# Kernel optimization log

Hardware: AMD Instinct MI355X
Metric: run time of the kernel (lower is better)

## Reference

```python
import jax, jax.numpy as jnp
import numpy as np

B, T, H, PRED = 16384, 8, 256, 12


def _cell(x, h, c, Wih, Whh, bih, bhh):
    # PyTorch LSTM gate order: i, f, g, o
    g = x @ Wih.T + h @ Whh.T + bih + bhh
    i, f, gg, o = jnp.split(g, 4, axis=-1)
    c = jax.nn.sigmoid(f) * c + jax.nn.sigmoid(i) * jnp.tanh(gg)
    h = jax.nn.sigmoid(o) * jnp.tanh(c)
    return h, c


def _run_seq(x, layers):
    # stacked LSTM over full sequence, zero initial state; x: [B, T, D]
    b = x.shape[0]
    inp = x
    hs, cs = [], []
    for (Wih, Whh, bih, bhh) in layers:
        h0 = jnp.zeros((b, Whh.shape[1]), x.dtype)

        def step(carry, xt, Wih=Wih, Whh=Whh, bih=bih, bhh=bhh):
            h, c = _cell(xt, carry[0], carry[1], Wih, Whh, bih, bhh)
            return (h, c), h

        (h, c), out = jax.lax.scan(step, (h0, h0), jnp.swapaxes(inp, 0, 1))
        inp = jnp.swapaxes(out, 0, 1)
        hs.append(h)
        cs.append(c)
    return inp, jnp.stack(hs), jnp.stack(cs)


def _step_stack(x, hs, cs, layers):
    # single-timestep pass through stacked LSTM; hs/cs: [L, B, H]
    inp = x
    nh, nc = [], []
    for l, (Wih, Whh, bih, bhh) in enumerate(layers):
        h, c = _cell(inp, hs[l], cs[l], Wih, Whh, bih, bhh)
        inp = h
        nh.append(h)
        nc.append(c)
    return inp, jnp.stack(nh), jnp.stack(nc)


def _forward(x, l1_Wih0, l1_Whh0, l1_bih0, l1_bhh0, l1_Wih1, l1_Whh1, l1_bih1, l1_bhh1,
             l2_Wih0, l2_Whh0, l2_bih0, l2_bhh0, l2_Wih1, l2_Whh1, l2_bih1, l2_bhh1,
             fc1_w, fc1_b, fc2_w, fc2_b):
    L1 = [(l1_Wih0, l1_Whh0, l1_bih0, l1_bhh0), (l1_Wih1, l1_Whh1, l1_bih1, l1_bhh1)]
    L2 = [(l2_Wih0, l2_Whh0, l2_bih0, l2_bhh0), (l2_Wih1, l2_Whh1, l2_bih1, l2_bhh1)]
    out1, h1, c1 = _run_seq(x, L1)           # encode observed track
    _, h2, c2 = _run_seq(out1, L2)
    pos = x[:, -1, :]

    def dec(carry, _):
        pos, h1, c1, h2, c2 = carry
        o1, h1, c1 = _step_stack(pos, h1, c1, L1)
        o2, h2, c2 = _step_stack(o1, h2, c2, L2)
        delta = jax.nn.relu(o2 @ fc1_w.T + fc1_b) @ fc2_w.T + fc2_b
        pos = pos + delta
        return (pos, h1, c1, h2, c2), pos

    _, preds = jax.lax.scan(dec, (pos, h1, c1, h2, c2), None, length=PRED)
    return jnp.swapaxes(preds, 0, 1)  # [B, PRED, 2]


def setup_inputs() -> dict:
    key = jax.random.key(0)
    ks = iter(jax.random.split(key, 32))
    s = 1.0 / np.sqrt(H)  # matches PyTorch LSTM/Linear init scale

    def mk(shape):
        return jax.random.uniform(next(ks), shape, jnp.float32, -s, s)

    d = {"x": jax.random.normal(next(ks), (B, T, 2), jnp.float32)}
    for name, in_dim in [("l1", 2), ("l2", H)]:
        for layer in range(2):
            di = in_dim if layer == 0 else H
            d[f"{name}_Wih{layer}"] = mk((4 * H, di))
            d[f"{name}_Whh{layer}"] = mk((4 * H, H))
            d[f"{name}_bih{layer}"] = mk((4 * H,))
            d[f"{name}_bhh{layer}"] = mk((4 * H,))
    d["fc1_w"] = mk((H, H))
    d["fc1_b"] = mk((H,))
    d["fc2_w"] = mk((2, H))
    d["fc2_b"] = mk((2,))
    return d


def reference(x, l1_Wih0, l1_Whh0, l1_bih0, l1_bhh0, l1_Wih1, l1_Whh1, l1_bih1, l1_bhh1,
              l2_Wih0, l2_Whh0, l2_bih0, l2_bhh0, l2_Wih1, l2_Whh1, l2_bih1, l2_bhh1,
              fc1_w, fc1_b, fc2_w, fc2_b):
    return _forward(x, l1_Wih0, l1_Whh0, l1_bih0, l1_bhh0, l1_Wih1, l1_Whh1, l1_bih1, l1_bhh1,
                    l2_Wih0, l2_Whh0, l2_bih0, l2_bhh0, l2_Wih1, l2_Whh1, l2_bih1, l2_bhh1,
                    fc1_w, fc1_b, fc2_w, fc2_b)
```

## Files before the change

### kernel.cpp

```cpp
#include <hip/hip_runtime.h>
#include <stdint.h>

#define Bsz   16384
#define Tseq  8
#define NPRED 12

typedef __attribute__((ext_vector_type(4))) float    f32x4;
typedef _Float16 h16;
typedef __attribute__((ext_vector_type(8))) _Float16 h16x8;

__device__ __forceinline__ float sigf(float x)   { return 1.f / (1.f + __expf(-x)); }
__device__ __forceinline__ float tanh_f(float x) { return 1.f - 2.f / (__expf(2.f * x) + 1.f); }

__device__ __forceinline__ void gload_lds16(const void* g, void* l) {
  __builtin_amdgcn_global_load_lds(
      (const __attribute__((address_space(1))) void*)g,
      (__attribute__((address_space(3))) void*)l, 16, 0, 0);
}

__global__ void zero_r8(f32x4* __restrict__ p, long n4) {
  long i = (long)blockIdx.x * 256 + threadIdx.x;
  f32x4 z; z[0] = 0.f; z[1] = 0.f; z[2] = 0.f; z[3] = 0.f;
  if (i < n4) p[i] = z;
}
__global__ void mark_r8(float* __restrict__ out) {
  if (blockIdx.x == 0 && threadIdx.x < 64) out[threadIdx.x] = 1000.0f;
}
__global__ void seed_r8(float* __restrict__ pos, const float* __restrict__ x) {
  int b = blockIdx.x * 256 + threadIdx.x;
  pos[2 * b]     = x[(size_t)b * 16 + 14];
  pos[2 * b + 1] = x[(size_t)b * 16 + 15];
}

__global__ void pack_w(h16* __restrict__ dst, const float* __restrict__ W0,
                       const float* __restrict__ W1, int ksplit, int Kw, int Np,
                       int gatePack) {
  int idx = blockIdx.x * 256 + threadIdx.x;
  if (idx >= Np * Kw) return;
  int np = idx / Kw, k = idx - np * Kw;
  int n = np;
  if (gatePack) { int jb = np >> 7, gi = (np >> 5) & 3, jr = np & 31; n = gi * 256 + jb * 32 + jr; }
  float w = (k < ksplit) ? W0[(size_t)n * ksplit + k]
                         : W1[(size_t)n * (Kw - ksplit) + (k - ksplit)];
  uint32_t byte = (uint32_t)np * (uint32_t)(Kw * 2) + (((uint32_t)k * 2) ^ (uint32_t)((np & 7) << 4));
  *(h16*)((char*)dst + byte) = (h16)w;
}

__global__ void add_bias(float* __restrict__ dst, const float* __restrict__ a,
                         const float* __restrict__ b) {
  int i = blockIdx.x * 256 + threadIdx.x;
  if (i < 1024) dst[i] = a[i] + b[i];
}

template <int NSEG, int HASX, int LSTM>
__global__ __launch_bounds__(256, 4) void cell_gemm(
    const char* __restrict__ A0, const char* __restrict__ A1,
    const char* __restrict__ Wp, int Kw, int NY,
    const float* __restrict__ bias, const float* __restrict__ wih0,
    const float* __restrict__ xbase, int xstride,
    float* __restrict__ Cst, char* __restrict__ hout) {
  __shared__ __align__(16) char lds[32768];
  char* ldsA = lds;
  char* ldsB = lds + 16384;
  const int tid = threadIdx.x;
  const int wave = tid >> 6, lane = tid & 63;

  int lid = blockIdx.x;
  int chunkv = gridDim.x >> 3;
  int swz = (lid & 7) * chunkv + (lid >> 3);
  const int by = swz % NY, bx = swz / NY;
  const int m0 = bx * 128;
  const int n0 = by * 128;

  f32x4 acc[2][8];
#pragma unroll
  for (int m = 0; m < 2; m++)
#pragma unroll
    for (int n = 0; n < 8; n++)
#pragma unroll
      for (int e = 0; e < 4; e++) acc[m][n][e] = 0.f;

  const int rowa = tid >> 3;
  const int chb  = (tid & 7) * 16;
  const int KB   = Kw >> 6;

  for (int kb = 0; kb < KB; ++kb) {
    const char* Asrc; int k0;
    if (NSEG == 2 && kb >= 4) { Asrc = A1; k0 = (kb - 4) << 6; }
    else                      { Asrc = A0; k0 = kb << 6; }
#pragma unroll
    for (int it = 0; it < 4; ++it) {
      gload_lds16(Asrc + (size_t)(m0 + it * 32 + rowa) * 512 + k0 * 2 + chb,
                  ldsA + it * 4096 + wave * 1024);
      gload_lds16(Wp + (size_t)(n0 + it * 32 + rowa) * (Kw * 2) + kb * 128 + chb,
                  ldsB + it * 4096 + wave * 1024);
    }
    __syncthreads();
#pragma unroll
    for (int kk = 0; kk < 2; ++kk) {
      const int kbyte = kk * 64 + (lane >> 4) * 16;
      h16x8 af[2];
#pragma unroll
      for (int mt = 0; mt < 2; ++mt) {
        int r = wave * 32 + mt * 16 + (lane & 15);
        af[mt] = *(const h16x8*)(ldsA + r * 128 + (kbyte ^ ((r & 7) << 4)));
      }
#pragma unroll
      for (int nh = 0; nh < 2; ++nh) {
        h16x8 bfr[4];
#pragma unroll
        for (int n4 = 0; n4 < 4; ++n4) {
          int cc = (nh * 4 + n4) * 16 + (lane & 15);
          bfr[n4] = *(const h16x8*)(ldsB + cc * 128 + (kbyte ^ ((cc & 7) << 4)));
        }
#pragma unroll
        for (int mt = 0; mt < 2; ++mt)
#pragma unroll
          for (int n4 = 0; n4 < 4; ++n4)
            acc[mt][nh * 4 + n4] =
                __builtin_amdgcn_mfma_f32_16x16x32_f16(af[mt], bfr[n4], acc[mt][nh * 4 + n4], 0, 0, 0);
      }
    }
    __syncthreads();
  }

  if constexpr (LSTM) {
#pragma unroll
    for (int c = 0; c < 2; c++) {
      const int j = (n0 >> 2) + c * 16 + (lane & 15);
      const float bi = bias[j], bff = bias[256 + j], bg = bias[512 + j], bo = bias[768 + j];
      float wi0 = 0, wi1 = 0, wf0 = 0, wf1 = 0, wg0 = 0, wg1 = 0, wo0 = 0, wo1 = 0;
      if constexpr (HASX) {
        wi0 = wih0[2 * j];           wi1 = wih0[2 * j + 1];
        wf0 = wih0[2 * (256 + j)];   wf1 = wih0[2 * (256 + j) + 1];
        wg0 = wih0[2 * (512 + j)];   wg1 = wih0[2 * (512 + j) + 1];
        wo0 = wih0[2 * (768 + j)];   wo1 = wih0[2 * (768 + j) + 1];
      }
#pragma unroll
      for (int mt = 0; mt < 2; ++mt) {
#pragma unroll
        for (int e = 0; e < 4; e++) {
          const int b = m0 + wave * 32 + mt * 16 + (lane >> 4) * 4 + e;
          float vi = acc[mt][0 + c][e] + bi;
          float vf = acc[mt][2 + c][e] + bff;
          float vg = acc[mt][4 + c][e] + bg;
          float vo = acc[mt][6 + c][e] + bo;
          if constexpr (HASX) {
            const float x0 = xbase[(size_t)b * xstride];
            const float x1 = xbase[(size_t)b * xstride + 1];
            vi += x0 * wi0 + x1 * wi1;
            vf += x0 * wf0 + x1 * wf1;
            vg += x0 * wg0 + x1 * wg1;
            vo += x0 * wo0 + x1 * wo1;
          }
          const size_t ci = (size_t)b * 256 + j;
          float cn = sigf(vf) * Cst[ci] + sigf(vi) * tanh_f(vg);
          float h  = sigf(vo) * tanh_f(cn);
          Cst[ci] = cn;
          *(h16*)(hout + (size_t)b * 512 + (((unsigned)j * 2) ^ (unsigned)((b & 7) << 4))) = (h16)h;
        }
      }
    }
  } else {
#pragma unroll
    for (int nt = 0; nt < 8; ++nt) {
      const int n = n0 + nt * 16 + (lane & 15);
      const float bn = bias[n];
#pragma unroll
      for (int mt = 0; mt < 2; ++mt)
#pragma unroll
        for (int e = 0; e < 4; e++) {
          const int b = m0 + wave * 32 + mt * 16 + (lane >> 4) * 4 + e;
          float v = acc[mt][nt][e] + bn;
          v = v > 0.f ? v : 0.f;
          *(h16*)(hout + (size_t)b * 512 + (((unsigned)n * 2) ^ (unsigned)((b & 7) << 4))) = (h16)v;
        }
    }
  }
}

__global__ void fc2_pos(const char* __restrict__ r, const float* __restrict__ w,
                        const float* __restrict__ fb, float* __restrict__ pos,
                        float* __restrict__ out, int s) {
  int b = blockIdx.x * 256 + threadIdx.x;
  float a0 = fb[0], a1 = fb[1];
#pragma unroll
  for (int ch = 0; ch < 32; ch++) {
    h16x8 v = *(const h16x8*)(r + (size_t)b * 512 + (((unsigned)ch * 16) ^ (unsigned)((b & 7) << 4)));
#pragma unroll
    for (int e = 0; e < 8; e++) {
      float rv = (float)v[e];
      int k = ch * 8 + e;
      a0 += rv * w[k];
      a1 += rv * w[256 + k];
    }
  }
  float p0 = pos[2 * b] + a0;
  float p1 = pos[2 * b + 1] + a1;
  pos[2 * b] = p0;
  pos[2 * b + 1] = p1;
  out[(size_t)b * (NPRED * 2) + s * 2]     = p0;
  out[(size_t)b * (NPRED * 2) + s * 2 + 1] = p1;
}

extern "C" void kernel_launch(void* const* d_in, const int* in_sizes, int n_in,
                              void* d_out, int out_size, void* d_ws, size_t ws_size,
                              hipStream_t stream) {
  const float* x      = (const float*)d_in[0];
  const float* Wih[4] = {(const float*)d_in[1], (const float*)d_in[5],
                         (const float*)d_in[9], (const float*)d_in[13]};
  const float* Whh[4] = {(const float*)d_in[2], (const float*)d_in[6],
                         (const float*)d_in[10], (const float*)d_in[14]};
  const float* bih[4] = {(const float*)d_in[3], (const float*)d_in[7],
                         (const float*)d_in[11], (const float*)d_in[15]};
  const float* bhh[4] = {(const float*)d_in[4], (const float*)d_in[8],
                         (const float*)d_in[12], (const float*)d_in[16]};
  const float* fc1_w = (const float*)d_in[17];
  const float* fc1_b = (const float*)d_in[18];
  const float* fc2_w = (const float*)d_in[19];
  const float* fc2_b = (const float*)d_in[20];

  char* ws = (char*)d_ws;
  size_t off = 0;
  auto alloc = [&](size_t bytes) -> char* {
    char* p = ws + off;
    off += (bytes + 255) & ~(size_t)255;
    return p;
  };

  float* Cs[4];
  for (int l = 0; l < 4; l++) Cs[l] = (float*)alloc((size_t)Bsz * 256 * 4);
  char* zeroh = alloc((size_t)Bsz * 512);
  char* h10[2] = {alloc((size_t)Bsz * 512), alloc((size_t)Bsz * 512)};
  char* sl[2]  = {alloc((size_t)Bsz * 512), alloc((size_t)Bsz * 512)};
  char* h20[2] = {alloc((size_t)Bsz * 512), alloc((size_t)Bsz * 512)};
  char* h21[2] = {alloc((size_t)Bsz * 512), alloc((size_t)Bsz * 512)};
  char* rbuf = alloc((size_t)Bsz * 512);
  float* pos = (float*)alloc((size_t)Bsz * 2 * 4);
  float* biasc = (float*)alloc(4 * 1024 * 4);
  h16* wp10 = (h16*)alloc((size_t)1024 * 256 * 2);
  h16* wp[3];
  for (int i = 0; i < 3; i++) wp[i] = (h16*)alloc((size_t)1024 * 512 * 2);
  h16* wpf1 = (h16*)alloc((size_t)256 * 256 * 2);

  if (ws_size < off) {
    mark_r8<<<dim3(1), dim3(64), 0, stream>>>((float*)d_out);
    return;
  }

  {
    long n4 = ((size_t)Bsz * 256 * 4 * 4 + (size_t)Bsz * 512) / 16;
    zero_r8<<<dim3((unsigned)((n4 + 255) / 256)), dim3(256), 0, stream>>>((f32x4*)Cs[0], n4);
  }
  seed_r8<<<dim3(Bsz / 256), dim3(256), 0, stream>>>(pos, x);

  pack_w<<<dim3((1024 * 256 + 255) / 256), dim3(256), 0, stream>>>(wp10, Whh[0], Whh[0], 256, 256, 1024, 1);
  pack_w<<<dim3((1024 * 512 + 255) / 256), dim3(256), 0, stream>>>(wp[0], Wih[1], Whh[1], 256, 512, 1024, 1);
  pack_w<<<dim3((1024 * 512 + 255) / 256), dim3(256), 0, stream>>>(wp[1], Wih[2], Whh[2], 256, 512, 1024, 1);
  pack_w<<<dim3((1024 * 512 + 255) / 256), dim3(256), 0, stream>>>(wp[2], Wih[3], Whh[3], 256, 512, 1024, 1);
  pack_w<<<dim3((256 * 256 + 255) / 256), dim3(256), 0, stream>>>(wpf1, fc1_w, fc1_w, 256, 256, 256, 0);
  for (int l = 0; l < 4; l++)
    add_bias<<<dim3(4), dim3(256), 0, stream>>>(biasc + l * 1024, bih[l], bhh[l]);

  for (int t = 0; t < Tseq; t++) {
    int cur = t & 1, prev = cur ^ 1;
    const char* h10r = (t == 0) ? zeroh : h10[prev];
    const char* slr  = (t == 0) ? zeroh : sl[prev];
    const char* h20r = (t == 0) ? zeroh : h20[prev];
    const char* h21r = (t == 0) ? zeroh : h21[prev];
    cell_gemm<1, 1, 1><<<dim3(1024), dim3(256), 0, stream>>>(
        h10r, zeroh, (const char*)wp10, 256, 8, biasc, Wih[0], x + t * 2, 16, Cs[0], h10[cur]);
    cell_gemm<2, 0, 1><<<dim3(1024), dim3(256), 0, stream>>>(
        h10[cur], slr, (const char*)wp[0], 512, 8, biasc + 1024, nullptr, nullptr, 0, Cs[1], sl[cur]);
    cell_gemm<2, 0, 1><<<dim3(1024), dim3(256), 0, stream>>>(
        sl[cur], h20r, (const char*)wp[1], 512, 8, biasc + 2048, nullptr, nullptr, 0, Cs[2], h20[cur]);
    cell_gemm<2, 0, 1><<<dim3(1024), dim3(256), 0, stream>>>(
        h20[cur], h21r, (const char*)wp[2], 512, 8, biasc + 3072, nullptr, nullptr, 0, Cs[3], h21[cur]);
  }

  for (int s = 0; s < NPRED; s++) {
    int u = Tseq + s, cur = u & 1, prev = cur ^ 1;
    cell_gemm<1, 1, 1><<<dim3(1024), dim3(256), 0, stream>>>(
        h10[prev], zeroh, (const char*)wp10, 256, 8, biasc, Wih[0], pos, 2, Cs[0], h10[cur]);
    cell_gemm<2, 0, 1><<<dim3(1024), dim3(256), 0, stream>>>(
        h10[cur], sl[prev], (const char*)wp[0], 512, 8, biasc + 1024, nullptr, nullptr, 0, Cs[1], sl[cur]);
    cell_gemm<2, 0, 1><<<dim3(1024), dim3(256), 0, stream>>>(
        sl[cur], h20[prev], (const char*)wp[1], 512, 8, biasc + 2048, nullptr, nullptr, 0, Cs[2], h20[cur]);
    cell_gemm<2, 0, 1><<<dim3(1024), dim3(256), 0, stream>>>(
        h20[cur], h21[prev], (const char*)wp[2], 512, 8, biasc + 3072, nullptr, nullptr, 0, Cs[3], h21[cur]);
    cell_gemm<1, 0, 0><<<dim3(256), dim3(256), 0, stream>>>(
        h21[cur], zeroh, (const char*)wpf1, 256, 2, fc1_b, nullptr, nullptr, 0, nullptr, rbuf);
    fc2_pos<<<dim3(Bsz / 256), dim3(256), 0, stream>>>(rbuf, fc2_w, fc2_b, pos, (float*)d_out, s);
  }
}
```

Measured before the change: 2.772 ms.

## Run encoder LSTM cells in diagonal wavefront with one fused launch per diagonal

Replaces the 32 sequential per-cell encoder launches with 11 wavefront launches. Each launch runs all (layer, timestep) cells on one anti-diagonal, using a descriptor array indexed by blockIdx. This cuts launch count and lets independent cells of different layers run at the same time, so the GPU has up to four times as many blocks per launch. Double-buffered h tensors are indexed by t parity, which must stay correct when different layers at different timesteps share a launch. Kernel helpers are also renamed.

```diff
diff --git a/kernel.cpp b/kernel.cpp
--- a/kernel.cpp
+++ b/kernel.cpp
@@ -18,15 +18,15 @@
       (__attribute__((address_space(3))) void*)l, 16, 0, 0);
 }
 
-__global__ void zero_r8(f32x4* __restrict__ p, long n4) {
+__global__ void zero_r9(f32x4* __restrict__ p, long n4) {
   long i = (long)blockIdx.x * 256 + threadIdx.x;
   f32x4 z; z[0] = 0.f; z[1] = 0.f; z[2] = 0.f; z[3] = 0.f;
   if (i < n4) p[i] = z;
 }
-__global__ void mark_r8(float* __restrict__ out) {
+__global__ void mark_r9(float* __restrict__ out) {
   if (blockIdx.x == 0 && threadIdx.x < 64) out[threadIdx.x] = 1000.0f;
 }
-__global__ void seed_r8(float* __restrict__ pos, const float* __restrict__ x) {
+__global__ void seed_r9(float* __restrict__ pos, const float* __restrict__ x) {
   int b = blockIdx.x * 256 + threadIdx.x;
   pos[2 * b]     = x[(size_t)b * 16 + 14];
   pos[2 * b + 1] = x[(size_t)b * 16 + 15];
@@ -50,6 +50,121 @@
                          const float* __restrict__ b) {
   int i = blockIdx.x * 256 + threadIdx.x;
   if (i < 1024) dst[i] = a[i] + b[i];
+}
+
+struct CellDesc {
+  const char* A0; const char* A1; const char* Wp;
+  const float* bias; const float* wih0; const float* xbase;
+  float* Cst; char* hout;
+  int Kw; int xstride; int hasx;
+};
+struct Fused4 { CellDesc c[4]; };
+
+__global__ __launch_bounds__(256, 4) void cells_diag(Fused4 args) {
+  const int cellid = blockIdx.x >> 10;
+  const int lid    = blockIdx.x & 1023;
+  const CellDesc d = args.c[cellid];
+
+  __shared__ __align__(16) char lds[32768];
+  char* ldsA = lds;
+  char* ldsB = lds + 16384;
+  const int tid = threadIdx.x;
+  const int wave = tid >> 6, lane = tid & 63;
+
+  int swz = (lid & 7) * 128 + (lid >> 3);
+  const int by = swz & 7, bx = swz >> 3;
+  const int m0 = bx * 128;
+  const int n0 = by * 128;
+
+  f32x4 acc[2][8];
+#pragma unroll
+  for (int m = 0; m < 2; m++)
+#pragma unroll
+    for (int n = 0; n < 8; n++)
+#pragma unroll
+      for (int e = 0; e < 4; e++) acc[m][n][e] = 0.f;
+
+  const int rowa = tid >> 3;
+  const int chb  = (tid & 7) * 16;
+  const int KB   = d.Kw >> 6;
+  const size_t wrow = (size_t)(d.Kw * 2);
+
+  for (int kb = 0; kb < KB; ++kb) {
+    const char* Asrc; int k0;
+    if (kb >= 4) { Asrc = d.A1; k0 = (kb - 4) << 6; }
+    else         { Asrc = d.A0; k0 = kb << 6; }
+#pragma unroll
+    for (int it = 0; it < 4; ++it) {
+      gload_lds16(Asrc + (size_t)(m0 + it * 32 + rowa) * 512 + k0 * 2 + chb,
+                  ldsA + it * 4096 + wave * 1024);
+      gload_lds16(d.Wp + (size_t)(n0 + it * 32 + rowa) * wrow + kb * 128 + chb,
+                  ldsB + it * 4096 + wave * 1024);
+    }
+    __syncthreads();
+#pragma unroll
+    for (int kk = 0; kk < 2; ++kk) {
+      const int kbyte = kk * 64 + (lane >> 4) * 16;
+      h16x8 af[2];
+#pragma unroll
+      for (int mt = 0; mt < 2; ++mt) {
+        int r = wave * 32 + mt * 16 + (lane & 15);
+        af[mt] = *(const h16x8*)(ldsA + r * 128 + (kbyte ^ ((r & 7) << 4)));
+      }
+#pragma unroll
+      for (int nh = 0; nh < 2; ++nh) {
+        h16x8 bfr[4];
+#pragma unroll
+        for (int n4 = 0; n4 < 4; ++n4) {
+          int cc = (nh * 4 + n4) * 16 + (lane & 15);
+          bfr[n4] = *(const h16x8*)(ldsB + cc * 128 + (kbyte ^ ((cc & 7) << 4)));
+        }
+#pragma unroll
+        for (int mt = 0; mt < 2; ++mt)
+#pragma unroll
+          for (int n4 = 0; n4 < 4; ++n4)
+            acc[mt][nh * 4 + n4] =
+                __builtin_amdgcn_mfma_f32_16x16x32_f16(af[mt], bfr[n4], acc[mt][nh * 4 + n4], 0, 0, 0);
+      }
+    }
+    __syncthreads();
+  }
+
+#pragma unroll
+  for (int c = 0; c < 2; c++) {
+    const int j = (n0 >> 2) + c * 16 + (lane & 15);
+    const float bi = d.bias[j], bff = d.bias[256 + j], bg = d.bias[512 + j], bo = d.bias[768 + j];
+    float wi0 = 0, wi1 = 0, wf0 = 0, wf1 = 0, wg0 = 0, wg1 = 0, wo0 = 0, wo1 = 0;
+    if (d.hasx) {
+      wi0 = d.wih0[2 * j];           wi1 = d.wih0[2 * j + 1];
+      wf0 = d.wih0[2 * (256 + j)];   wf1 = d.wih0[2 * (256 + j) + 1];
+      wg0 = d.wih0[2 * (512 + j)];   wg1 = d.wih0[2 * (512 + j) + 1];
+      wo0 = d.wih0[2 * (768 + j)];   wo1 = d.wih0[2 * (768 + j) + 1];
+    }
+#pragma unroll
+    for (int mt = 0; mt < 2; ++mt) {
+#pragma unroll
+      for (int e = 0; e < 4; e++) {
+        const int b = m0 + wave * 32 + mt * 16 + (lane >> 4) * 4 + e;
+        float vi = acc[mt][0 + c][e] + bi;
+        float vf = acc[mt][2 + c][e] + bff;
+        float vg = acc[mt][4 + c][e] + bg;
+        float vo = acc[mt][6 + c][e] + bo;
+        if (d.hasx) {
+          const float x0 = d.xbase[(size_t)b * d.xstride];
+          const float x1 = d.xbase[(size_t)b * d.xstride + 1];
+          vi += x0 * wi0 + x1 * wi1;
+          vf += x0 * wf0 + x1 * wf1;
+          vg += x0 * wg0 + x1 * wg1;
+          vo += x0 * wo0 + x1 * wo1;
+        }
+        const size_t ci = (size_t)b * 256 + j;
+        float cn = sigf(vf) * d.Cst[ci] + sigf(vi) * tanh_f(vg);
+        float h  = sigf(vo) * tanh_f(cn);
+        d.Cst[ci] = cn;
+        *(h16*)(d.hout + (size_t)b * 512 + (((unsigned)j * 2) ^ (unsigned)((b & 7) << 4))) = (h16)h;
+      }
+    }
+  }
 }
 
 template <int NSEG, int HASX, int LSTM>
@@ -244,15 +359,15 @@
   h16* wpf1 = (h16*)alloc((size_t)256 * 256 * 2);
 
   if (ws_size < off) {
-    mark_r8<<<dim3(1), dim3(64), 0, stream>>>((float*)d_out);
+    mark_r9<<<dim3(1), dim3(64), 0, stream>>>((float*)d_out);
     return;
   }
 
   {
     long n4 = ((size_t)Bsz * 256 * 4 * 4 + (size_t)Bsz * 512) / 16;
-    zero_r8<<<dim3((unsigned)((n4 + 255) / 256)), dim3(256), 0, stream>>>((f32x4*)Cs[0], n4);
-  }
-  seed_r8<<<dim3(Bsz / 256), dim3(256), 0, stream>>>(pos, x);
+    zero_r9<<<dim3((unsigned)((n4 + 255) / 256)), dim3(256), 0, stream>>>((f32x4*)Cs[0], n4);
+  }
+  seed_r9<<<dim3(Bsz / 256), dim3(256), 0, stream>>>(pos, x);
 
   pack_w<<<dim3((1024 * 256 + 255) / 256), dim3(256), 0, stream>>>(wp10, Whh[0], Whh[0], 256, 256, 1024, 1);
   pack_w<<<dim3((1024 * 512 + 255) / 256), dim3(256), 0, stream>>>(wp[0], Wih[1], Whh[1], 256, 512, 1024, 1);
@@ -262,20 +377,30 @@
   for (int l = 0; l < 4; l++)
     add_bias<<<dim3(4), dim3(256), 0, stream>>>(biasc + l * 1024, bih[l], bhh[l]);
 
-  for (int t = 0; t < Tseq; t++) {
-    int cur = t & 1, prev = cur ^ 1;
-    const char* h10r = (t == 0) ? zeroh : h10[prev];
-    const char* slr  = (t == 0) ? zeroh : sl[prev];
-    const char* h20r = (t == 0) ? zeroh : h20[prev];
-    const char* h21r = (t == 0) ? zeroh : h21[prev];
-    cell_gemm<1, 1, 1><<<dim3(1024), dim3(256), 0, stream>>>(
-        h10r, zeroh, (const char*)wp10, 256, 8, biasc, Wih[0], x + t * 2, 16, Cs[0], h10[cur]);
-    cell_gemm<2, 0, 1><<<dim3(1024), dim3(256), 0, stream>>>(
-        h10[cur], slr, (const char*)wp[0], 512, 8, biasc + 1024, nullptr, nullptr, 0, Cs[1], sl[cur]);
-    cell_gemm<2, 0, 1><<<dim3(1024), dim3(256), 0, stream>>>(
-        sl[cur], h20r, (const char*)wp[1], 512, 8, biasc + 2048, nullptr, nullptr, 0, Cs[2], h20[cur]);
-    cell_gemm<2, 0, 1><<<dim3(1024), dim3(256), 0, stream>>>(
-        h20[cur], h21r, (const char*)wp[2], 512, 8, biasc + 3072, nullptr, nullptr, 0, Cs[3], h21[cur]);
+  char* hbuf[4][2] = {{h10[0], h10[1]}, {sl[0], sl[1]}, {h20[0], h20[1]}, {h21[0], h21[1]}};
+  const h16* wpl[4] = {wp10, wp[0], wp[1], wp[2]};
+  for (int d = 0; d <= 10; d++) {
+    Fused4 args;
+    int nc = 0;
+    for (int l = 0; l < 4; l++) {
+      int t = d - l;
+      if (t < 0 || t >= Tseq) continue;
+      CellDesc& cd = args.c[nc++];
+      cd.A0 = (l == 0) ? ((t == 0) ? zeroh : hbuf[0][(t - 1) & 1])
+                       : hbuf[l - 1][t & 1];
+      cd.A1 = (l == 0) ? zeroh
+                       : ((t == 0) ? zeroh : hbuf[l][(t - 1) & 1]);
+      cd.Wp = (const char*)wpl[l];
+      cd.bias = biasc + l * 1024;
+      cd.wih0 = (l == 0) ? Wih[0] : nullptr;
+      cd.xbase = (l == 0) ? (x + t * 2) : nullptr;
+      cd.Cst = Cs[l];
+      cd.hout = hbuf[l][t & 1];
+      cd.Kw = (l == 0) ? 256 : 512;
+      cd.xstride = 16;
+      cd.hasx = (l == 0) ? 1 : 0;
+    }
+    cells_diag<<<dim3(nc * 1024), dim3(256), 0, stream>>>(args);
   }
 
   for (int s = 0; s < NPRED; s++) {
```

After: 2.625 ms. 5.3% less time.
